# Kernel tuning notes

Measured on AMD Instinct MI355X. Metric: run time of the kernel, lower is better.

Reference implementation:

```python
import jax, jax.numpy as jnp
import numpy as np

N_NODES = 100000
N_EDGES = 1600000
D_IN, D_HID, D_OUT = 128, 128, 64


def setup_inputs() -> dict:
    key = jax.random.key(0)
    ks = jax.random.split(key, 6)
    x = jax.random.normal(ks[0], (N_NODES, D_IN), dtype=jnp.float32)
    edge_index = jax.random.randint(ks[1], (2, N_EDGES), 0, N_NODES, dtype=jnp.int64)
    s1 = 1.0 / np.sqrt(D_IN)
    s2 = 1.0 / np.sqrt(D_HID)
    return {
        "x": x,
        "edge_index": edge_index,
        "Wl1": jax.random.uniform(ks[2], (D_HID, D_IN), jnp.float32, -s1, s1),
        "bl1": jnp.zeros((D_HID,), jnp.float32),
        "Wr1": jax.random.uniform(ks[3], (D_HID, D_IN), jnp.float32, -s1, s1),
        "Wl2": jax.random.uniform(ks[4], (D_OUT, D_HID), jnp.float32, -s2, s2),
        "bl2": jnp.zeros((D_OUT,), jnp.float32),
        "Wr2": jax.random.uniform(ks[5], (D_OUT, D_HID), jnp.float32, -s2, s2),
    }


def _sage_conv(x, src, dst, Wl, bl, Wr, n_nodes):
    # mean-aggregate neighbor features src -> dst
    agg = jax.ops.segment_sum(x[src], dst, num_segments=n_nodes)  # [N, d_in]
    deg = jax.ops.segment_sum(jnp.ones((src.shape[0],), x.dtype), dst, num_segments=n_nodes)
    agg = agg / jnp.maximum(deg, 1.0)[:, None]
    # PyG SAGEConv: lin_l(agg) + lin_r(x), bias only on lin_l
    return agg @ Wl.T + bl + x @ Wr.T


def reference(x, edge_index, Wl1, bl1, Wr1, Wl2, bl2, Wr2):
    src, dst = edge_index[0], edge_index[1]
    n = x.shape[0]
    h = _sage_conv(x, src, dst, Wl1, bl1, Wr1, n)
    h = jax.nn.relu(h)
    # dropout is identity in eval mode (training=False)
    out = _sage_conv(h, src, dst, Wl2, bl2, Wr2, n)
    return out
```

## Files before the change

### kernel.cpp

```cpp
#include <hip/hip_runtime.h>

#define N_NODES_C 100000
#define N_EDGES_C 1600000
#define NT32_C 3125
#define NBUCK_C 392
#define BCAP_C 4800
#define EPB_C 2048

typedef _Float16 half_t;
typedef __attribute__((ext_vector_type(2))) _Float16 half2v;
typedef __attribute__((ext_vector_type(8))) _Float16 half8v;
typedef __attribute__((ext_vector_type(4))) float floatx4;

#if defined(__has_builtin)
#if __has_builtin(__builtin_amdgcn_fdot2)
#define HAS_FDOT2 1
#endif
#endif

__global__ void bucket_kernel(const int* __restrict__ src, const int* __restrict__ dst,
                              int* __restrict__ gcur, int* __restrict__ bucket, int E) {
    __shared__ int lcnt[NBUCK_C];
    __shared__ int lbase[NBUCK_C];
    __shared__ int lcur[NBUCK_C];
    const int tid = threadIdx.x;
    const int e0 = blockIdx.x * EPB_C;
    const int n = min(EPB_C, E - e0);

    for (int i = tid; i < NBUCK_C; i += 256) { lcnt[i] = 0; lcur[i] = 0; }
    __syncthreads();
    for (int i = tid; i < n; i += 256) {
        atomicAdd(&lcnt[dst[e0 + i] >> 8], 1);
    }
    __syncthreads();
    for (int i = tid; i < NBUCK_C; i += 256) {
        int c = lcnt[i];
        lbase[i] = (c > 0) ? atomicAdd(&gcur[i], c) : 0;
    }
    __syncthreads();
    for (int i = tid; i < n; i += 256) {
        int d = dst[e0 + i];
        int s = src[e0 + i];
        int b = d >> 8;
        int p = lbase[b] + atomicAdd(&lcur[b], 1);
        if (p < BCAP_C) bucket[b * BCAP_C + p] = (s << 8) | (d & 255);
    }
}

__global__ void csr_build_kernel(const int* __restrict__ gcur, const int* __restrict__ bucket,
                                 int2* __restrict__ nodeinfo, int* __restrict__ csr, int N) {
    __shared__ int sg[NBUCK_C];
    __shared__ int lcnt[256];
    __shared__ int lcur[256];
    __shared__ int sc[2][256];
    __shared__ int eord[BCAP_C];
    __shared__ int sbase_s;
    const int b = blockIdx.x;
    const int tid = threadIdx.x;
    const int ne = min(gcur[b], BCAP_C);

    for (int i = tid; i < NBUCK_C; i += 256) sg[i] = min(gcur[i], BCAP_C);
    lcnt[tid] = 0;
    lcur[tid] = 0;
    __syncthreads();
    if (tid == 0) {
        int s = 0;
        for (int i = 0; i < b; i++) s += sg[i];
        sbase_s = s;
    }
    const int* be = bucket + b * BCAP_C;
    for (int i = tid; i < ne; i += 256) {
        atomicAdd(&lcnt[be[i] & 255], 1);
    }
    __syncthreads();
    sc[0][tid] = lcnt[tid];
    __syncthreads();
    int cur = 0;
    for (int off = 1; off < 256; off <<= 1) {
        int v = sc[cur][tid] + ((tid >= off) ? sc[cur][tid - off] : 0);
        sc[1 - cur][tid] = v;
        __syncthreads();
        cur ^= 1;
    }
    for (int i = tid; i < ne; i += 256) {
        int p = be[i];
        int dl = p & 255;
        int slot = atomicAdd(&lcur[dl], 1);
        int pre = (dl == 0) ? 0 : sc[cur][dl - 1];
        eord[pre + slot] = p >> 8;
    }
    __syncthreads();
    const int sbase = sbase_s;
    for (int i = tid; i < ne; i += 256) csr[sbase + i] = eord[i];
    int node = (b << 8) + tid;
    if (node < N) {
        int pre = (tid == 0) ? 0 : sc[cur][tid - 1];
        nodeinfo[node] = make_int2(sbase + pre, lcnt[tid]);
    }
}

__global__ void prep_kernel(const float* __restrict__ Wl1, const float* __restrict__ Wr1,
                            const float* __restrict__ Wl2, const float* __restrict__ Wr2,
                            const float* __restrict__ x,
                            half_t* __restrict__ B1, half_t* __restrict__ B2,
                            half_t* __restrict__ xh) {
    int blk = blockIdx.x;
    int tid = threadIdx.x;
    if (blk < 128) {
        int t = blk * 256 + tid;
        int j  = t & 7;
        int l  = (t >> 3) & 63;
        int ks = (t >> 9) & 7;
        int ct = t >> 12;
        int k = ks * 32 + ((l >> 4) << 3) + j;
        int o = ct * 16 + (l & 15);
        float v = (k < 128) ? Wl1[o * 128 + k] : Wr1[o * 128 + (k - 128)];
        B1[t] = (half_t)v;
    } else if (blk < 192) {
        int t = (blk - 128) * 256 + tid;
        int j  = t & 7;
        int l  = (t >> 3) & 63;
        int ks = (t >> 9) & 3;
        int ct = t >> 11;
        int k = ks * 32 + ((l >> 4) << 3) + j;
        int o = ct * 16 + (l & 15);
        float v = (o < 64) ? Wl2[o * 128 + k] : Wr2[(o - 64) * 128 + k];
        B2[t] = (half_t)v;
    } else {
        int t = (blk - 192) * 256 + tid;
        if (t >= N_NODES_C * 16) return;
        const float4* p = (const float4*)x;
        float4 a = p[(size_t)t * 2];
        float4 b = p[(size_t)t * 2 + 1];
        half_t r[8] = {(half_t)a.x, (half_t)a.y, (half_t)a.z, (half_t)a.w,
                       (half_t)b.x, (half_t)b.y, (half_t)b.z, (half_t)b.w};
        *(uint4*)(xh + (size_t)t * 8) = *(uint4*)r;
    }
}

static __device__ __forceinline__ void dot8(float* a, uint4 v) {
    unsigned int u[4] = {v.x, v.y, v.z, v.w};
#ifdef HAS_FDOT2
    const half2v e0 = {(half_t)1.0f, (half_t)0.0f};
    const half2v e1 = {(half_t)0.0f, (half_t)1.0f};
#pragma unroll
    for (int i = 0; i < 4; i++) {
        union { unsigned int x; half2v h; } c; c.x = u[i];
        a[2 * i]     = __builtin_amdgcn_fdot2(c.h, e0, a[2 * i], false);
        a[2 * i + 1] = __builtin_amdgcn_fdot2(c.h, e1, a[2 * i + 1], false);
    }
#else
#pragma unroll
    for (int i = 0; i < 4; i++) {
        union { unsigned int x; half2v h; } c; c.x = u[i];
        a[2 * i]     += (float)c.h.x;
        a[2 * i + 1] += (float)c.h.y;
    }
#endif
}

static __device__ __forceinline__ void dot4(float* a, uint2 v) {
    unsigned int u[2] = {v.x, v.y};
#ifdef HAS_FDOT2
    const half2v e0 = {(half_t)1.0f, (half_t)0.0f};
    const half2v e1 = {(half_t)0.0f, (half_t)1.0f};
#pragma unroll
    for (int i = 0; i < 2; i++) {
        union { unsigned int x; half2v h; } c; c.x = u[i];
        a[2 * i]     = __builtin_amdgcn_fdot2(c.h, e0, a[2 * i], false);
        a[2 * i + 1] = __builtin_amdgcn_fdot2(c.h, e1, a[2 * i + 1], false);
    }
#else
#pragma unroll
    for (int i = 0; i < 2; i++) {
        union { unsigned int x; half2v h; } c; c.x = u[i];
        a[2 * i]     += (float)c.h.x;
        a[2 * i + 1] += (float)c.h.y;
    }
#endif
}

__global__ void agg1_kernel(const half_t* __restrict__ xh,
                            const int2* __restrict__ nodeinfo,
                            const int* __restrict__ csr,
                            half_t* __restrict__ aggh, int N) {
    int wid = (blockIdx.x * 256 + threadIdx.x) >> 6;
    if (wid >= N) return;
    int lane = threadIdx.x & 63;
    int q = lane >> 4;
    int c = lane & 15;
    int2 info = nodeinfo[wid];
    const int* row = csr + info.x;
    const int deg = info.y;
    float a0[8] = {0,0,0,0,0,0,0,0};
    float a1[8] = {0,0,0,0,0,0,0,0};
    int e = q;
    for (; e + 4 < deg; e += 8) {
        int s0 = row[e];
        int s1 = row[e + 4];
        uint4 v0 = *(const uint4*)(xh + (size_t)s0 * 128 + c * 8);
        uint4 v1 = *(const uint4*)(xh + (size_t)s1 * 128 + c * 8);
        dot8(a0, v0);
        dot8(a1, v1);
    }
    if (e < deg) {
        int s0 = row[e];
        uint4 v0 = *(const uint4*)(xh + (size_t)s0 * 128 + c * 8);
        dot8(a0, v0);
    }
    float acc[8];
#pragma unroll
    for (int j = 0; j < 8; j++) {
        float v = a0[j] + a1[j];
        v += __shfl_xor(v, 16, 64);
        v += __shfl_xor(v, 32, 64);
        acc[j] = v;
    }
    if (lane < 16) {
        float sc = 1.0f / fmaxf((float)deg, 1.0f);
        half_t r[8];
#pragma unroll
        for (int j = 0; j < 8; j++) r[j] = (half_t)(acc[j] * sc);
        *(uint4*)(aggh + (size_t)wid * 128 + c * 8) = *(uint4*)r;
    }
}

__launch_bounds__(256, 2)
__global__ void gemm1_kernel(const half_t* __restrict__ aggh,
                             const half_t* __restrict__ xh,
                             const half_t* __restrict__ B1,
                             const float* __restrict__ bias,
                             half_t* __restrict__ hh) {
    __shared__ half_t sA[32][264];

    const int wave = threadIdx.x >> 6;
    const int lane = threadIdx.x & 63;
    const int quad = lane >> 4;
    const int l16 = lane & 15;

    half8v bf[2][8];
    float bias_v[2];
#pragma unroll
    for (int i = 0; i < 2; i++) {
        int ct = wave * 2 + i;
        bias_v[i] = bias[ct * 16 + l16];
#pragma unroll
        for (int ks = 0; ks < 8; ks++) {
            bf[i][ks] = *(const half8v*)(B1 + ((ct * 8 + ks) * 64 + lane) * 8);
        }
    }

    const int tid = threadIdx.x;

    for (int tile = blockIdx.x; tile < NT32_C; tile += gridDim.x) {
        const int node0 = tile * 32;
        for (int u = tid; u < 512; u += 256) {
            int n = u >> 4, cc = u & 15;
            *(half8v*)&sA[n][cc * 8] =
                *(const half8v*)(aggh + (size_t)(node0 + n) * 128 + cc * 8);
            *(half8v*)&sA[n][128 + cc * 8] =
                *(const half8v*)(xh + (size_t)(node0 + n) * 128 + cc * 8);
        }
        __syncthreads();

        floatx4 acc[2][2];
#pragma unroll
        for (int i = 0; i < 2; i++)
#pragma unroll
            for (int s = 0; s < 2; s++)
                acc[i][s] = (floatx4){0.f, 0.f, 0.f, 0.f};

#pragma unroll
        for (int ks = 0; ks < 8; ks++) {
            half8v a0 = *(const half8v*)&sA[l16][ks * 32 + quad * 8];
            half8v a1 = *(const half8v*)&sA[16 + l16][ks * 32 + quad * 8];
#pragma unroll
            for (int i = 0; i < 2; i++) {
                acc[i][0] = __builtin_amdgcn_mfma_f32_16x16x32_f16(a0, bf[i][ks], acc[i][0], 0, 0, 0);
                acc[i][1] = __builtin_amdgcn_mfma_f32_16x16x32_f16(a1, bf[i][ks], acc[i][1], 0, 0, 0);
            }
        }

#pragma unroll
        for (int i = 0; i < 2; i++) {
            int o = wave * 32 + i * 16 + l16;
#pragma unroll
            for (int s = 0; s < 2; s++) {
                float vals[4] = {acc[i][s].x, acc[i][s].y, acc[i][s].z, acc[i][s].w};
#pragma unroll
                for (int r = 0; r < 4; r++) {
                    int node = node0 + s * 16 + quad * 4 + r;
                    float v = fmaxf(vals[r] + bias_v[i], 0.f);
                    hh[(size_t)node * 128 + o] = (half_t)v;
                }
            }
        }
        __syncthreads();
    }
}

__launch_bounds__(256, 2)
__global__ void gemm2_kernel(const half_t* __restrict__ hh,
                             const half_t* __restrict__ B2,
                             const float* __restrict__ bias,
                             half_t* __restrict__ g,
                             half_t* __restrict__ s2h) {
    __shared__ half_t sA[32][136];

    const int wave = threadIdx.x >> 6;
    const int lane = threadIdx.x & 63;
    const int quad = lane >> 4;
    const int l16 = lane & 15;

    half8v bf[2][4];
    float bias_v[2];
#pragma unroll
    for (int i = 0; i < 2; i++) {
        int ct = wave * 2 + i;
        int o = ct * 16 + l16;
        bias_v[i] = (o >= 64) ? bias[o - 64] : 0.f;
#pragma unroll
        for (int ks = 0; ks < 4; ks++) {
            bf[i][ks] = *(const half8v*)(B2 + ((ct * 4 + ks) * 64 + lane) * 8);
        }
    }

    const int tid = threadIdx.x;

    for (int tile = blockIdx.x; tile < NT32_C; tile += gridDim.x) {
        const int node0 = tile * 32;
        for (int u = tid; u < 512; u += 256) {
            int n = u >> 4, cc = u & 15;
            *(half8v*)&sA[n][cc * 8] =
                *(const half8v*)(hh + (size_t)(node0 + n) * 128 + cc * 8);
        }
        __syncthreads();

        floatx4 acc[2][2];
#pragma unroll
        for (int i = 0; i < 2; i++)
#pragma unroll
            for (int s = 0; s < 2; s++)
                acc[i][s] = (floatx4){0.f, 0.f, 0.f, 0.f};

#pragma unroll
        for (int ks = 0; ks < 4; ks++) {
            half8v a0 = *(const half8v*)&sA[l16][ks * 32 + quad * 8];
            half8v a1 = *(const half8v*)&sA[16 + l16][ks * 32 + quad * 8];
#pragma unroll
            for (int i = 0; i < 2; i++) {
                acc[i][0] = __builtin_amdgcn_mfma_f32_16x16x32_f16(a0, bf[i][ks], acc[i][0], 0, 0, 0);
                acc[i][1] = __builtin_amdgcn_mfma_f32_16x16x32_f16(a1, bf[i][ks], acc[i][1], 0, 0, 0);
            }
        }

#pragma unroll
        for (int i = 0; i < 2; i++) {
            int o = wave * 32 + i * 16 + l16;
#pragma unroll
            for (int s = 0; s < 2; s++) {
                float vals[4] = {acc[i][s].x, acc[i][s].y, acc[i][s].z, acc[i][s].w};
#pragma unroll
                for (int r = 0; r < 4; r++) {
                    int node = node0 + s * 16 + quad * 4 + r;
                    float v = vals[r] + bias_v[i];
                    if (o < 64) g[(size_t)node * 64 + o] = (half_t)v;
                    else        s2h[(size_t)node * 64 + (o - 64)] = (half_t)v;
                }
            }
        }
        __syncthreads();
    }
}

__global__ void agg2e_kernel(const half_t* __restrict__ g,
                             const half_t* __restrict__ s2h,
                             const int2* __restrict__ nodeinfo,
                             const int* __restrict__ csr,
                             float* __restrict__ out, int N) {
    int wid = (blockIdx.x * 256 + threadIdx.x) >> 6;
    if (wid >= N) return;
    int lane = threadIdx.x & 63;
    int q = lane >> 4;
    int c = lane & 15;
    int2 info = nodeinfo[wid];
    const int* row = csr + info.x;
    const int deg = info.y;
    float a0[4] = {0,0,0,0};
    float a1[4] = {0,0,0,0};
    int e = q;
    for (; e + 4 < deg; e += 8) {
        int s0 = row[e];
        int s1 = row[e + 4];
        uint2 v0 = *(const uint2*)(g + (size_t)s0 * 64 + c * 4);
        uint2 v1 = *(const uint2*)(g + (size_t)s1 * 64 + c * 4);
        dot4(a0, v0);
        dot4(a1, v1);
    }
    if (e < deg) {
        int s0 = row[e];
        uint2 v0 = *(const uint2*)(g + (size_t)s0 * 64 + c * 4);
        dot4(a0, v0);
    }
    float acc[4];
#pragma unroll
    for (int j = 0; j < 4; j++) {
        float v = a0[j] + a1[j];
        v += __shfl_xor(v, 16, 64);
        v += __shfl_xor(v, 32, 64);
        acc[j] = v;
    }
    if (lane < 16) {
        float sc = 1.0f / fmaxf((float)deg, 1.0f);
        uint2 sv = *(const uint2*)(s2h + (size_t)wid * 64 + c * 4);
        union { unsigned int x; half2v h; } c0, c1;
        c0.x = sv.x; c1.x = sv.y;
        float4 r;
        r.x = acc[0] * sc + (float)c0.h.x;
        r.y = acc[1] * sc + (float)c0.h.y;
        r.z = acc[2] * sc + (float)c1.h.x;
        r.w = acc[3] * sc + (float)c1.h.y;
        *(float4*)(out + (size_t)wid * 64 + c * 4) = r;
    }
}

extern "C" void kernel_launch(void* const* d_in, const int* in_sizes, int n_in,
                              void* d_out, int out_size, void* d_ws, size_t ws_size,
                              hipStream_t stream) {
    const float* x    = (const float*)d_in[0];
    const int*   ei   = (const int*)d_in[1];
    const float* Wl1  = (const float*)d_in[2];
    const float* bl1  = (const float*)d_in[3];
    const float* Wr1  = (const float*)d_in[4];
    const float* Wl2  = (const float*)d_in[5];
    const float* bl2  = (const float*)d_in[6];
    const float* Wr2  = (const float*)d_in[7];
    float* out = (float*)d_out;

    const int N = N_NODES_C;
    const int E = N_EDGES_C;
    const int* src = ei;
    const int* dst = ei + E;

    char* ws = (char*)d_ws;
    half_t* B1   = (half_t*)(ws + 0);
    half_t* B2   = (half_t*)(ws + 65536);
    int*    gcur = (int*)   (ws + 98304);
    int2*   nodeinfo = (int2*)(ws + 102400);
    int*    csr  = (int*)   (ws + 1048576);
    half_t* xh   = (half_t*)(ws + 7448576);
    half_t* aggh = (half_t*)(ws + 33048576);
    half_t* hh   = (half_t*)(ws + 58648576);
    half_t* g    = aggh;
    half_t* s2h  = aggh + 6400000;
    int*    bucket = (int*)hh;

    hipMemsetAsync(gcur, 0, NBUCK_C * sizeof(int), stream);
    bucket_kernel<<<(E + EPB_C - 1) / EPB_C, 256, 0, stream>>>(src, dst, gcur, bucket, E);
    csr_build_kernel<<<NBUCK_C, 256, 0, stream>>>(gcur, bucket, nodeinfo, csr, N);

    prep_kernel<<<192 + (N * 16 + 255) / 256, 256, 0, stream>>>(
        Wl1, Wr1, Wl2, Wr2, x, B1, B2, xh);

    agg1_kernel<<<(N + 3) / 4, 256, 0, stream>>>(xh, nodeinfo, csr, aggh, N);
    gemm1_kernel<<<512, 256, 0, stream>>>(aggh, xh, B1, bl1, hh);

    gemm2_kernel<<<512, 256, 0, stream>>>(hh, B2, bl2, g, s2h);
    agg2e_kernel<<<(N + 3) / 4, 256, 0, stream>>>(g, s2h, nodeinfo, csr, out, N);
}
```

Before: 294.0 us.

## Fuse layer-1 neighbor aggregation into GEMM kernel and widen agg2 loads

Layer-1 mean aggregation moves into the GEMM kernel: each block gathers neighbor features for its 32 nodes straight into shared memory and then runs the MFMA GEMM. This removes the aggh round trip through global memory and one kernel launch. Separately, the layer-2 aggregation now uses 8 lanes per row with 16-byte loads and 8 edges in flight per wave, at the cost of one extra shuffle stage. The fused kernel launches one block per tile and loses the persistent loop, and its occupancy is now capped by the GEMM's register and shared-memory use during the latency-bound gather.

```diff
diff --git a/kernel.cpp b/kernel.cpp
--- a/kernel.cpp
+++ b/kernel.cpp
@@ -159,84 +159,64 @@
 #endif
 }
 
-static __device__ __forceinline__ void dot4(float* a, uint2 v) {
-    unsigned int u[2] = {v.x, v.y};
-#ifdef HAS_FDOT2
-    const half2v e0 = {(half_t)1.0f, (half_t)0.0f};
-    const half2v e1 = {(half_t)0.0f, (half_t)1.0f};
-#pragma unroll
-    for (int i = 0; i < 2; i++) {
-        union { unsigned int x; half2v h; } c; c.x = u[i];
-        a[2 * i]     = __builtin_amdgcn_fdot2(c.h, e0, a[2 * i], false);
-        a[2 * i + 1] = __builtin_amdgcn_fdot2(c.h, e1, a[2 * i + 1], false);
-    }
-#else
-#pragma unroll
-    for (int i = 0; i < 2; i++) {
-        union { unsigned int x; half2v h; } c; c.x = u[i];
-        a[2 * i]     += (float)c.h.x;
-        a[2 * i + 1] += (float)c.h.y;
-    }
-#endif
-}
-
-__global__ void agg1_kernel(const half_t* __restrict__ xh,
-                            const int2* __restrict__ nodeinfo,
-                            const int* __restrict__ csr,
-                            half_t* __restrict__ aggh, int N) {
-    int wid = (blockIdx.x * 256 + threadIdx.x) >> 6;
-    if (wid >= N) return;
-    int lane = threadIdx.x & 63;
-    int q = lane >> 4;
-    int c = lane & 15;
-    int2 info = nodeinfo[wid];
-    const int* row = csr + info.x;
-    const int deg = info.y;
-    float a0[8] = {0,0,0,0,0,0,0,0};
-    float a1[8] = {0,0,0,0,0,0,0,0};
-    int e = q;
-    for (; e + 4 < deg; e += 8) {
-        int s0 = row[e];
-        int s1 = row[e + 4];
-        uint4 v0 = *(const uint4*)(xh + (size_t)s0 * 128 + c * 8);
-        uint4 v1 = *(const uint4*)(xh + (size_t)s1 * 128 + c * 8);
-        dot8(a0, v0);
-        dot8(a1, v1);
-    }
-    if (e < deg) {
-        int s0 = row[e];
-        uint4 v0 = *(const uint4*)(xh + (size_t)s0 * 128 + c * 8);
-        dot8(a0, v0);
-    }
-    float acc[8];
-#pragma unroll
-    for (int j = 0; j < 8; j++) {
-        float v = a0[j] + a1[j];
-        v += __shfl_xor(v, 16, 64);
-        v += __shfl_xor(v, 32, 64);
-        acc[j] = v;
-    }
-    if (lane < 16) {
-        float sc = 1.0f / fmaxf((float)deg, 1.0f);
-        half_t r[8];
-#pragma unroll
-        for (int j = 0; j < 8; j++) r[j] = (half_t)(acc[j] * sc);
-        *(uint4*)(aggh + (size_t)wid * 128 + c * 8) = *(uint4*)r;
-    }
-}
-
 __launch_bounds__(256, 2)
-__global__ void gemm1_kernel(const half_t* __restrict__ aggh,
-                             const half_t* __restrict__ xh,
-                             const half_t* __restrict__ B1,
-                             const float* __restrict__ bias,
-                             half_t* __restrict__ hh) {
+__global__ void l1_kernel(const half_t* __restrict__ xh,
+                          const int2* __restrict__ nodeinfo,
+                          const int* __restrict__ csr,
+                          const half_t* __restrict__ B1,
+                          const float* __restrict__ bias,
+                          half_t* __restrict__ hh) {
     __shared__ half_t sA[32][264];
 
     const int wave = threadIdx.x >> 6;
     const int lane = threadIdx.x & 63;
     const int quad = lane >> 4;
     const int l16 = lane & 15;
+    const int tid = threadIdx.x;
+    const int node0 = blockIdx.x * 32;
+
+    for (int u = tid; u < 512; u += 256) {
+        int n = u >> 4, cc = u & 15;
+        *(half8v*)&sA[n][128 + cc * 8] =
+            *(const half8v*)(xh + (size_t)(node0 + n) * 128 + cc * 8);
+    }
+
+    for (int i = 0; i < 8; i++) {
+        const int n = wave * 8 + i;
+        const int2 info = nodeinfo[node0 + n];
+        const int* row = csr + info.x;
+        const int deg = info.y;
+        float a0[8] = {0,0,0,0,0,0,0,0};
+        float a1[8] = {0,0,0,0,0,0,0,0};
+        int e = quad;
+        for (; e + 4 < deg; e += 8) {
+            int s0 = row[e];
+            int s1 = row[e + 4];
+            uint4 v0 = *(const uint4*)(xh + (size_t)s0 * 128 + l16 * 8);
+            uint4 v1 = *(const uint4*)(xh + (size_t)s1 * 128 + l16 * 8);
+            dot8(a0, v0);
+            dot8(a1, v1);
+        }
+        if (e < deg) {
+            uint4 v0 = *(const uint4*)(xh + (size_t)row[e] * 128 + l16 * 8);
+            dot8(a0, v0);
+        }
+        float sc = 1.0f / fmaxf((float)deg, 1.0f);
+#pragma unroll
+        for (int j = 0; j < 8; j++) {
+            float v = a0[j] + a1[j];
+            v += __shfl_xor(v, 16, 64);
+            v += __shfl_xor(v, 32, 64);
+            a0[j] = v * sc;
+        }
+        if (lane < 16) {
+            half_t r[8];
+#pragma unroll
+            for (int j = 0; j < 8; j++) r[j] = (half_t)a0[j];
+            *(uint4*)&sA[n][l16 * 8] = *(uint4*)r;
+        }
+    }
+    __syncthreads();
 
     half8v bf[2][8];
     float bias_v[2];
@@ -250,52 +230,37 @@
         }
     }
 
-    const int tid = threadIdx.x;
-
-    for (int tile = blockIdx.x; tile < NT32_C; tile += gridDim.x) {
-        const int node0 = tile * 32;
-        for (int u = tid; u < 512; u += 256) {
-            int n = u >> 4, cc = u & 15;
-            *(half8v*)&sA[n][cc * 8] =
-                *(const half8v*)(aggh + (size_t)(node0 + n) * 128 + cc * 8);
-            *(half8v*)&sA[n][128 + cc * 8] =
-                *(const half8v*)(xh + (size_t)(node0 + n) * 128 + cc * 8);
-        }
-        __syncthreads();
-
-        floatx4 acc[2][2];
-#pragma unroll
-        for (int i = 0; i < 2; i++)
-#pragma unroll
-            for (int s = 0; s < 2; s++)
-                acc[i][s] = (floatx4){0.f, 0.f, 0.f, 0.f};
-
-#pragma unroll
-        for (int ks = 0; ks < 8; ks++) {
-            half8v a0 = *(const half8v*)&sA[l16][ks * 32 + quad * 8];
-            half8v a1 = *(const half8v*)&sA[16 + l16][ks * 32 + quad * 8];
-#pragma unroll
-            for (int i = 0; i < 2; i++) {
-                acc[i][0] = __builtin_amdgcn_mfma_f32_16x16x32_f16(a0, bf[i][ks], acc[i][0], 0, 0, 0);
-                acc[i][1] = __builtin_amdgcn_mfma_f32_16x16x32_f16(a1, bf[i][ks], acc[i][1], 0, 0, 0);
+    floatx4 acc[2][2];
+#pragma unroll
+    for (int i = 0; i < 2; i++)
+#pragma unroll
+        for (int s = 0; s < 2; s++)
+            acc[i][s] = (floatx4){0.f, 0.f, 0.f, 0.f};
+
+#pragma unroll
+    for (int ks = 0; ks < 8; ks++) {
+        half8v a0 = *(const half8v*)&sA[l16][ks * 32 + quad * 8];
+        half8v a1 = *(const half8v*)&sA[16 + l16][ks * 32 + quad * 8];
+#pragma unroll
+        for (int i = 0; i < 2; i++) {
+            acc[i][0] = __builtin_amdgcn_mfma_f32_16x16x32_f16(a0, bf[i][ks], acc[i][0], 0, 0, 0);
+            acc[i][1] = __builtin_amdgcn_mfma_f32_16x16x32_f16(a1, bf[i][ks], acc[i][1], 0, 0, 0);
+        }
+    }
+
+#pragma unroll
+    for (int i = 0; i < 2; i++) {
+        int o = wave * 32 + i * 16 + l16;
+#pragma unroll
+        for (int s = 0; s < 2; s++) {
+            float vals[4] = {acc[i][s].x, acc[i][s].y, acc[i][s].z, acc[i][s].w};
+#pragma unroll
+            for (int r = 0; r < 4; r++) {
+                int node = node0 + s * 16 + quad * 4 + r;
+                float v = fmaxf(vals[r] + bias_v[i], 0.f);
+                hh[(size_t)node * 128 + o] = (half_t)v;
             }
         }
-
-#pragma unroll
-        for (int i = 0; i < 2; i++) {
-            int o = wave * 32 + i * 16 + l16;
-#pragma unroll
-            for (int s = 0; s < 2; s++) {
-                float vals[4] = {acc[i][s].x, acc[i][s].y, acc[i][s].z, acc[i][s].w};
-#pragma unroll
-                for (int r = 0; r < 4; r++) {
-                    int node = node0 + s * 16 + quad * 4 + r;
-                    float v = fmaxf(vals[r] + bias_v[i], 0.f);
-                    hh[(size_t)node * 128 + o] = (half_t)v;
-                }
-            }
-        }
-        __syncthreads();
     }
 }
 
@@ -381,46 +346,51 @@
     int wid = (blockIdx.x * 256 + threadIdx.x) >> 6;
     if (wid >= N) return;
     int lane = threadIdx.x & 63;
-    int q = lane >> 4;
-    int c = lane & 15;
+    int q = lane >> 3;
+    int c = lane & 7;
     int2 info = nodeinfo[wid];
     const int* row = csr + info.x;
     const int deg = info.y;
-    float a0[4] = {0,0,0,0};
-    float a1[4] = {0,0,0,0};
+    float a0[8] = {0,0,0,0,0,0,0,0};
+    float a1[8] = {0,0,0,0,0,0,0,0};
     int e = q;
-    for (; e + 4 < deg; e += 8) {
+    for (; e + 8 < deg; e += 16) {
         int s0 = row[e];
-        int s1 = row[e + 4];
-        uint2 v0 = *(const uint2*)(g + (size_t)s0 * 64 + c * 4);
-        uint2 v1 = *(const uint2*)(g + (size_t)s1 * 64 + c * 4);
-        dot4(a0, v0);
-        dot4(a1, v1);
+        int s1 = row[e + 8];
+        uint4 v0 = *(const uint4*)(g + (size_t)s0 * 64 + c * 8);
+        uint4 v1 = *(const uint4*)(g + (size_t)s1 * 64 + c * 8);
+        dot8(a0, v0);
+        dot8(a1, v1);
     }
     if (e < deg) {
-        int s0 = row[e];
-        uint2 v0 = *(const uint2*)(g + (size_t)s0 * 64 + c * 4);
-        dot4(a0, v0);
-    }
-    float acc[4];
-#pragma unroll
-    for (int j = 0; j < 4; j++) {
+        uint4 v0 = *(const uint4*)(g + (size_t)row[e] * 64 + c * 8);
+        dot8(a0, v0);
+    }
+    float acc[8];
+#pragma unroll
+    for (int j = 0; j < 8; j++) {
         float v = a0[j] + a1[j];
+        v += __shfl_xor(v, 8, 64);
         v += __shfl_xor(v, 16, 64);
         v += __shfl_xor(v, 32, 64);
         acc[j] = v;
     }
-    if (lane < 16) {
+    if (lane < 8) {
         float sc = 1.0f / fmaxf((float)deg, 1.0f);
-        uint2 sv = *(const uint2*)(s2h + (size_t)wid * 64 + c * 4);
-        union { unsigned int x; half2v h; } c0, c1;
-        c0.x = sv.x; c1.x = sv.y;
-        float4 r;
-        r.x = acc[0] * sc + (float)c0.h.x;
-        r.y = acc[1] * sc + (float)c0.h.y;
-        r.z = acc[2] * sc + (float)c1.h.x;
-        r.w = acc[3] * sc + (float)c1.h.y;
-        *(float4*)(out + (size_t)wid * 64 + c * 4) = r;
+        uint4 sv = *(const uint4*)(s2h + (size_t)wid * 64 + c * 8);
+        union { unsigned int x; half2v h; } c0, c1, c2, c3;
+        c0.x = sv.x; c1.x = sv.y; c2.x = sv.z; c3.x = sv.w;
+        float4 r0, r1;
+        r0.x = acc[0] * sc + (float)c0.h.x;
+        r0.y = acc[1] * sc + (float)c0.h.y;
+        r0.z = acc[2] * sc + (float)c1.h.x;
+        r0.w = acc[3] * sc + (float)c1.h.y;
+        r1.x = acc[4] * sc + (float)c2.h.x;
+        r1.y = acc[5] * sc + (float)c2.h.y;
+        r1.z = acc[6] * sc + (float)c3.h.x;
+        r1.w = acc[7] * sc + (float)c3.h.y;
+        *(float4*)(out + (size_t)wid * 64 + c * 8) = r0;
+        *(float4*)(out + (size_t)wid * 64 + c * 8 + 4) = r1;
     }
 }
 
@@ -462,8 +432,7 @@
     prep_kernel<<<192 + (N * 16 + 255) / 256, 256, 0, stream>>>(
         Wl1, Wr1, Wl2, Wr2, x, B1, B2, xh);
 
-    agg1_kernel<<<(N + 3) / 4, 256, 0, stream>>>(xh, nodeinfo, csr, aggh, N);
-    gemm1_kernel<<<512, 256, 0, stream>>>(aggh, xh, B1, bl1, hh);
+    l1_kernel<<<NT32_C, 256, 0, stream>>>(xh, nodeinfo, csr, B1, bl1, hh);
 
     gemm2_kernel<<<512, 256, 0, stream>>>(hh, B2, bl2, g, s2h);
     agg2e_kernel<<<(N + 3) / 4, 256, 0, stream>>>(g, s2h, nodeinfo, csr, out, N);
```

Measured after the change: 278.7 us. 5.2% less time.
